# Kernel tuning notes

Hardware: AMD Instinct MI355X
Metric: run time of the kernel (lower is better)

## Reference

```python
import jax, jax.numpy as jnp
import numpy as np

DIM = 32
N_TOKENS = 4
HIDDEN = 2 * DIM
BATCH = 262144
EPS = 1e-5
SCALE = 1.0 / float(np.sqrt(DIM))


def _ln(x, g, b):
    m = jnp.mean(x, axis=-1, keepdims=True)
    v = jnp.mean((x - m) ** 2, axis=-1, keepdims=True)
    return (x - m) * jax.lax.rsqrt(v + EPS) * g + b


def setup_inputs() -> dict:
    key = jax.random.key(0)
    ks = jax.random.split(key, 16)
    s = 0.02
    lin = lambda k, i, o: jax.random.normal(k, (i, o), jnp.float32) * s
    return {
        "x": jax.random.normal(ks[0], (BATCH, N_TOKENS, DIM), jnp.float32),
        "w_pe": lin(ks[1], DIM, DIM),
        "b_pe": jnp.zeros((DIM,), jnp.float32),
        "pos": jax.random.normal(ks[2], (1, N_TOKENS, DIM), jnp.float32) * s,
        "ln1_g": jnp.ones((DIM,), jnp.float32),
        "ln1_b": jnp.zeros((DIM,), jnp.float32),
        "wq": lin(ks[3], DIM, DIM), "bq": jnp.zeros((DIM,), jnp.float32),
        "wk": lin(ks[4], DIM, DIM), "bk": jnp.zeros((DIM,), jnp.float32),
        "wv": lin(ks[5], DIM, DIM), "bv": jnp.zeros((DIM,), jnp.float32),
        "wo": lin(ks[6], DIM, DIM), "bo": jnp.zeros((DIM,), jnp.float32),
        "ln2_g": jnp.ones((DIM,), jnp.float32),
        "ln2_b": jnp.zeros((DIM,), jnp.float32),
        "w1": lin(ks[7], DIM, HIDDEN), "bf1": jnp.zeros((HIDDEN,), jnp.float32),
        "w2": lin(ks[8], HIDDEN, DIM), "bf2": jnp.zeros((DIM,), jnp.float32),
    }


def reference(x, w_pe, b_pe, pos, ln1_g, ln1_b, wq, bq, wk, bk, wv, bv,
              wo, bo, ln2_g, ln2_b, w1, bf1, w2, bf2):
    # patch embed + positional embedding
    x = x @ w_pe + b_pe + pos                      # [B, T, D]
    # attention block
    xa = _ln(x, ln1_g, ln1_b)
    q = xa @ wq + bq
    k = xa @ wk + bk
    v = xa @ wv + bv
    scores = jnp.einsum("btd,bsd->bts", q, k) * SCALE  # [B, T, T]
    attn = jax.nn.softmax(scores, axis=-1)
    mixed = jnp.einsum("bts,bsd->btd", attn, v)
    x = x + mixed @ wo + bo
    # MLP block (gelu tanh approximation, matching F.gelu(approximate='tanh'))
    xb = _ln(x, ln2_g, ln2_b)
    h = jax.nn.gelu(xb @ w1 + bf1, approximate=True)   # [B, T, 2D]
    x = x + h @ w2 + bf2
    return x
```

## Files before the change

### kernel.cpp

```cpp
#include <hip/hip_runtime.h>
#include <hip/hip_bf16.h>

typedef float          f32x4  __attribute__((ext_vector_type(4)));
typedef __bf16         bf16x8 __attribute__((ext_vector_type(8)));
typedef unsigned short u16x8  __attribute__((ext_vector_type(8)));
typedef unsigned int   u32;

#define DEV static __device__ __forceinline__

static constexpr int   NT      = 65536;
static constexpr float SCALE_Q = 0.17677669529663687f;
static constexpr float LOG2E   = 1.44269504f;

DEV unsigned short f2bf(float f) {
  return __builtin_bit_cast(unsigned short, __float2bfloat16(f));
}
DEV u32 pk2(float lo, float hi) { return (u32)f2bf(lo) | ((u32)f2bf(hi) << 16); }

DEV u16x8 pack8(f32x4 a, f32x4 b) {
  uint4 q;
  q.x = pk2(a[0], a[1]); q.y = pk2(a[2], a[3]);
  q.z = pk2(b[0], b[1]); q.w = pk2(b[2], b[3]);
  return __builtin_bit_cast(u16x8, q);
}

DEV f32x4 mfma(u16x8 a, u16x8 b, f32x4 c) {
  return __builtin_amdgcn_mfma_f32_16x16x32_bf16(
      __builtin_bit_cast(bf16x8, a), __builtin_bit_cast(bf16x8, b), c, 0, 0, 0);
}
DEV void wait_lds() {
  asm volatile("s_waitcnt lgkmcnt(0)" ::: "memory");
  __builtin_amdgcn_sched_barrier(0);
}

DEV u16x8 build_frag(const float* W, int N, int k0, int col, float scale) {
  u16x8 f;
#pragma unroll
  for (int e = 0; e < 8; ++e)
    f[e] = f2bf(W[(k0 + e) * N + col] * scale);
  return f;
}
DEV u16x8 fold_frag(u16x8 f, const float* gv) {
  u16x8 o;
#pragma unroll
  for (int e = 0; e < 8; ++e) {
    union { u32 i; float v; } u; u.i = ((u32)f[e]) << 16;
    o[e] = f2bf(u.v * gv[e]);
  }
  return o;
}

DEV u16x8 conv_std(u32* buf, int r15, int lg, f32x4 a0, f32x4 a1) {
  const int wb = r15 * 20 + 2 * lg;
  buf[wb + 0] = pk2(a0[0], a0[1]);
  buf[wb + 1] = pk2(a0[2], a0[3]);
  buf[wb + 8] = pk2(a1[0], a1[1]);
  buf[wb + 9] = pk2(a1[2], a1[3]);
  wait_lds();
  uint4 rd = *(const uint4*)(buf + r15 * 20 + 4 * lg);
  return __builtin_bit_cast(u16x8, rd);
}

DEV void ln_stats(f32x4 a, f32x4 b, float& rs, float& nm) {
  float s1 = 0.f, s2 = 0.f;
#pragma unroll
  for (int i = 0; i < 4; ++i) { s1 += a[i]; s2 = fmaf(a[i], a[i], s2); }
#pragma unroll
  for (int i = 0; i < 4; ++i) { s1 += b[i]; s2 = fmaf(b[i], b[i], s2); }
  s1 += __shfl_xor(s1, 16); s2 += __shfl_xor(s2, 16);
  s1 += __shfl_xor(s1, 32); s2 += __shfl_xor(s2, 32);
  const float m   = s1 * 0.03125f;
  const float var = fmaf(s2, 0.03125f, -m * m);
  rs = __builtin_amdgcn_rsqf(var + 1e-5f);
  nm = -m * rs;
}

DEV float gelu_t(float u) {
  const float u2 = u * u;
  float z2 = u * fmaf(u2, 0.07135481f, 1.59576912f);
  z2 = fminf(z2, 80.f);
  const float e = __builtin_amdgcn_exp2f(z2 * LOG2E);
  return u * e * __builtin_amdgcn_rcpf(e + 1.0f);
}

__global__ __launch_bounds__(256, 2) void vit_fused(
    const float* __restrict__ x,
    const float* __restrict__ wpe, const float* __restrict__ bpe,
    const float* __restrict__ pos,
    const float* __restrict__ ln1g, const float* __restrict__ ln1b,
    const float* __restrict__ wq, const float* __restrict__ bq,
    const float* __restrict__ wk, const float* __restrict__ bk,
    const float* __restrict__ wv, const float* __restrict__ bv,
    const float* __restrict__ wo, const float* __restrict__ bo,
    const float* __restrict__ ln2g, const float* __restrict__ ln2b,
    const float* __restrict__ w1, const float* __restrict__ bf1,
    const float* __restrict__ w2, const float* __restrict__ bf2,
    float* __restrict__ out) {
  const int tid = (int)threadIdx.x;
  const int wid = tid >> 6;
  const int l   = tid & 63;
  const int r15 = l & 15;
  const int lg  = l >> 4;
  const int tk  = l & 3;

  __shared__ alignas(16) u32   s_conv[4][2][320];
  __shared__ alignas(16) float s_q[4][576];
  __shared__ alignas(16) float s_k[4][576];
  __shared__ alignas(16) float s_vv[4][576];
  __shared__ alignas(16) float s_at[4][64];
  __shared__ alignas(16) u32   s_h[4][576];
  u32*   bufA = s_conv[wid][0];
  u32*   bufB = s_conv[wid][1];
  float* qS   = s_q[wid];
  float* kS   = s_k[wid];
  float* vS   = s_vv[wid];
  float* aT   = s_at[wid];
  u32*   hB   = s_h[wid];

  float g1v[8], g2v[8];
#pragma unroll
  for (int e = 0; e < 8; ++e) { g1v[e] = ln1g[8 * lg + e]; g2v[e] = ln2g[8 * lg + e]; }
  const u16x8 b1f = pack8(*(const f32x4*)(ln1b + 8 * lg), *(const f32x4*)(ln1b + 8 * lg + 4));
  const u16x8 b2f = pack8(*(const f32x4*)(ln2b + 8 * lg), *(const f32x4*)(ln2b + 8 * lg + 4));

  u16x8 wpeF[2], wqF[2], wkF[2], wvF[2], woF[2], w1F[4], w2F[2][2];
  f32x4 comboC[2], bqC[2], bkC[2], bvC[2], boC[2], bf2C[2], bf1C[4];

#pragma unroll
  for (int H = 0; H < 2; ++H) {
    const int dc  = 16 * H + 4 * lg;
    const int col = 16 * H + r15;
    wpeF[H]   = build_frag(wpe, 32, 8 * lg, col, 1.f);
    woF[H]    = build_frag(wo,  32, 8 * lg, col, 1.f);
    w2F[0][H] = build_frag(w2,  32, 8 * lg,      col, 1.f);
    w2F[1][H] = build_frag(w2,  32, 32 + 8 * lg, col, 1.f);
    f32x4 cq, ck, cv, cmb, cbo, cb2;
#pragma unroll
    for (int i = 0; i < 4; ++i) {
      const int d = dc + i;
      cmb[i] = bpe[d] + pos[tk * 32 + d];
      cq[i]  = SCALE_Q * bq[d];
      ck[i]  = bk[d];
      cv[i]  = bv[d];
      cbo[i] = bo[d];
      cb2[i] = bf2[d];
    }
    comboC[H] = cmb; boC[H] = cbo; bf2C[H] = cb2;
    const u16x8 rq = build_frag(wq, 32, 8 * lg, col, SCALE_Q);
    const u16x8 rk = build_frag(wk, 32, 8 * lg, col, 1.f);
    const u16x8 rv = build_frag(wv, 32, 8 * lg, col, 1.f);
    bqC[H] = mfma(rq, b1f, cq);
    bkC[H] = mfma(rk, b1f, ck);
    bvC[H] = mfma(rv, b1f, cv);
    wqF[H] = fold_frag(rq, g1v);
    wkF[H] = fold_frag(rk, g1v);
    wvF[H] = fold_frag(rv, g1v);
  }
#pragma unroll
  for (int Hp = 0; Hp < 4; ++Hp) {
    const int col = 16 * Hp + r15;
    const u16x8 r1 = build_frag(w1, 64, 8 * lg, col, 1.f);
    f32x4 c1;
#pragma unroll
    for (int i = 0; i < 4; ++i) c1[i] = bf1[16 * Hp + 4 * lg + i];
    bf1C[Hp] = mfma(r1, b2f, c1);
    w1F[Hp]  = fold_frag(r1, g2v);
  }

  const f32x4 zero4 = {0.f, 0.f, 0.f, 0.f};
  const int stride = (int)(gridDim.x << 2);
  int tile = (int)(blockIdx.x << 2) | wid;

  const float* xp = x + (size_t)(tile * 16 + r15) * 32 + 8 * lg;
  f32x4 xv0 = *(const f32x4*)(xp);
  f32x4 xv1 = *(const f32x4*)(xp + 4);
  for (; tile < NT; tile += stride) {
    const int nxt = tile + stride;
    f32x4 nx0 = xv0, nx1 = xv1;
    if (nxt < NT) {
      const float* np_ = x + (size_t)(nxt * 16 + r15) * 32 + 8 * lg;
      nx0 = *(const f32x4*)(np_);
      nx1 = *(const f32x4*)(np_ + 4);
    }
    const u16x8 xf = pack8(xv0, xv1);

    f32x4 x1a = mfma(wpeF[0], xf, comboC[0]);
    f32x4 x1b = mfma(wpeF[1], xf, comboC[1]);

    float rs, nm;
    ln_stats(x1a, x1b, rs, nm);
    f32x4 ya, yb;
#pragma unroll
    for (int i = 0; i < 4; ++i) { ya[i] = fmaf(x1a[i], rs, nm); yb[i] = fmaf(x1b[i], rs, nm); }
    const u16x8 xaf = conv_std(bufA, r15, lg, ya, yb);

    const f32x4 qa0 = mfma(wqF[0], xaf, bqC[0]);
    const f32x4 qa1 = mfma(wqF[1], xaf, bqC[1]);
    const f32x4 ka0 = mfma(wkF[0], xaf, bkC[0]);
    const f32x4 ka1 = mfma(wkF[1], xaf, bkC[1]);
    const f32x4 va0 = mfma(wvF[0], xaf, bvC[0]);
    const f32x4 va1 = mfma(wvF[1], xaf, bvC[1]);

    *(f32x4*)(qS + r15 * 36 + 4 * lg)      = qa0;
    *(f32x4*)(qS + r15 * 36 + 16 + 4 * lg) = qa1;
    *(f32x4*)(kS + r15 * 36 + 4 * lg)      = ka0;
    *(f32x4*)(kS + r15 * 36 + 16 + 4 * lg) = ka1;
    *(f32x4*)(vS + r15 * 36 + 4 * lg)      = va0;
    *(f32x4*)(vS + r15 * 36 + 16 + 4 * lg) = va1;
    wait_lds();

    const int qr = l >> 2;
    const int kr = (qr & 12) | (l & 3);
    float sc = 0.f;
#pragma unroll
    for (int c = 0; c < 8; ++c) {
      const f32x4 qv = *(const f32x4*)(qS + qr * 36 + 4 * c);
      const f32x4 kv = *(const f32x4*)(kS + kr * 36 + 4 * c);
      sc = fmaf(qv[0], kv[0], sc); sc = fmaf(qv[1], kv[1], sc);
      sc = fmaf(qv[2], kv[2], sc); sc = fmaf(qv[3], kv[3], sc);
    }
    float t0 = fmaxf(sc, __shfl_xor(sc, 1));
    const float mx = fmaxf(t0, __shfl_xor(t0, 2));
    const float ex = __builtin_amdgcn_exp2f((sc - mx) * LOG2E);
    float se = ex + __shfl_xor(ex, 1);
    se = se + __shfl_xor(se, 2);
    aT[l] = ex * __builtin_amdgcn_rcpf(se);
    wait_lds();

    const f32x4 atv = *(const f32x4*)(aT + (r15 << 2));
    f32x4 m0 = zero4, m1 = zero4;
#pragma unroll
    for (int j = 0; j < 4; ++j) {
      const f32x4 v0 = *(const f32x4*)(vS + ((r15 & 12) + j) * 36 + 4 * lg);
      const f32x4 v1 = *(const f32x4*)(vS + ((r15 & 12) + j) * 36 + 16 + 4 * lg);
      m0 += atv[j] * v0;
      m1 += atv[j] * v1;
    }
    const u16x8 mf = conv_std(bufB, r15, lg, m0, m1);

    const f32x4 x2a = mfma(woF[0], mf, x1a) + boC[0];
    const f32x4 x2b = mfma(woF[1], mf, x1b) + boC[1];

    ln_stats(x2a, x2b, rs, nm);
#pragma unroll
    for (int i = 0; i < 4; ++i) { ya[i] = fmaf(x2a[i], rs, nm); yb[i] = fmaf(x2b[i], rs, nm); }
    const u16x8 xbf = conv_std(bufA, r15, lg, ya, yb);

#pragma unroll
    for (int Hp = 0; Hp < 4; ++Hp) {
      const f32x4 h = mfma(w1F[Hp], xbf, bf1C[Hp]);
      const int hb = r15 * 36 + 8 * Hp + 2 * lg;
      hB[hb]     = pk2(gelu_t(h[0]), gelu_t(h[1]));
      hB[hb + 1] = pk2(gelu_t(h[2]), gelu_t(h[3]));
    }
    wait_lds();
    const uint4 h0r = *(const uint4*)(hB + r15 * 36 + 4 * lg);
    const uint4 h1r = *(const uint4*)(hB + r15 * 36 + 16 + 4 * lg);
    const u16x8 hf0 = __builtin_bit_cast(u16x8, h0r);
    const u16x8 hf1 = __builtin_bit_cast(u16x8, h1r);

    f32x4 o0 = x2a + bf2C[0];
    f32x4 o1 = x2b + bf2C[1];
    o0 = mfma(w2F[0][0], hf0, o0);
    o0 = mfma(w2F[1][0], hf1, o0);
    o1 = mfma(w2F[0][1], hf0, o1);
    o1 = mfma(w2F[1][1], hf1, o1);

    float* op = out + (size_t)(tile * 16 + r15) * 32;
    *(f32x4*)(op + 4 * lg)      = o0;
    *(f32x4*)(op + 16 + 4 * lg) = o1;

    xv0 = nx0; xv1 = nx1;
  }
}

extern "C" void kernel_launch(void* const* d_in, const int* in_sizes, int n_in,
                              void* d_out, int out_size, void* d_ws, size_t ws_size,
                              hipStream_t stream) {
  (void)in_sizes; (void)n_in; (void)d_ws; (void)ws_size; (void)out_size;
  const float* x    = (const float*)d_in[0];
  const float* wpe  = (const float*)d_in[1];
  const float* bpe  = (const float*)d_in[2];
  const float* pos  = (const float*)d_in[3];
  const float* ln1g = (const float*)d_in[4];
  const float* ln1b = (const float*)d_in[5];
  const float* wq   = (const float*)d_in[6];
  const float* bq   = (const float*)d_in[7];
  const float* wk   = (const float*)d_in[8];
  const float* bk   = (const float*)d_in[9];
  const float* wv   = (const float*)d_in[10];
  const float* bv   = (const float*)d_in[11];
  const float* wo   = (const float*)d_in[12];
  const float* bo   = (const float*)d_in[13];
  const float* ln2g = (const float*)d_in[14];
  const float* ln2b = (const float*)d_in[15];
  const float* w1   = (const float*)d_in[16];
  const float* bf1  = (const float*)d_in[17];
  const float* w2   = (const float*)d_in[18];
  const float* bf2  = (const float*)d_in[19];

  vit_fused<<<512, 256, 0, stream>>>(x, wpe, bpe, pos, ln1g, ln1b, wq, bq, wk, bk,
                                     wv, bv, wo, bo, ln2g, ln2b, w1, bf1, w2, bf2,
                                     (float*)d_out);
}
```

Baseline: 93.44 us.

## Compute attention scores with MFMA and shrink LDS to raise occupancy

Q and K are converted to bf16 fragments through the LDS conversion buffers, and the 16x16 score tile comes from one MFMA instead of scalar FMA dot products over fp32 LDS copies. Softmax over each 4-token group now runs in registers without cross-lane shuffles. The q/k LDS arrays are dropped, V and the hidden buffer share one array, launch bounds go to 4 blocks per CU, and the grid doubles to 1024 blocks. Scores are now computed in bf16 rather than fp32, which costs some precision, and the higher occupancy target may push registers toward spilling.

```diff
diff --git a/kernel.cpp b/kernel.cpp
--- a/kernel.cpp
+++ b/kernel.cpp
@@ -61,6 +61,23 @@
   return __builtin_bit_cast(u16x8, rd);
 }
 
+DEV void conv_qk(u32* bq_, u32* bk_, int r15, int lg,
+                 f32x4 q0, f32x4 q1, f32x4 k0, f32x4 k1,
+                 u16x8& qf, u16x8& kf) {
+  const int wb = r15 * 20 + 2 * lg;
+  bq_[wb + 0] = pk2(q0[0], q0[1]);
+  bq_[wb + 1] = pk2(q0[2], q0[3]);
+  bq_[wb + 8] = pk2(q1[0], q1[1]);
+  bq_[wb + 9] = pk2(q1[2], q1[3]);
+  bk_[wb + 0] = pk2(k0[0], k0[1]);
+  bk_[wb + 1] = pk2(k0[2], k0[3]);
+  bk_[wb + 8] = pk2(k1[0], k1[1]);
+  bk_[wb + 9] = pk2(k1[2], k1[3]);
+  wait_lds();
+  qf = __builtin_bit_cast(u16x8, *(const uint4*)(bq_ + r15 * 20 + 4 * lg));
+  kf = __builtin_bit_cast(u16x8, *(const uint4*)(bk_ + r15 * 20 + 4 * lg));
+}
+
 DEV void ln_stats(f32x4 a, f32x4 b, float& rs, float& nm) {
   float s1 = 0.f, s2 = 0.f;
 #pragma unroll
@@ -83,7 +100,7 @@
   return u * e * __builtin_amdgcn_rcpf(e + 1.0f);
 }
 
-__global__ __launch_bounds__(256, 2) void vit_fused(
+__global__ __launch_bounds__(256, 4) void vit_fused(
     const float* __restrict__ x,
     const float* __restrict__ wpe, const float* __restrict__ bpe,
     const float* __restrict__ pos,
@@ -104,18 +121,13 @@
   const int tk  = l & 3;
 
   __shared__ alignas(16) u32   s_conv[4][2][320];
-  __shared__ alignas(16) float s_q[4][576];
-  __shared__ alignas(16) float s_k[4][576];
-  __shared__ alignas(16) float s_vv[4][576];
+  __shared__ alignas(16) float s_vh[4][576];
   __shared__ alignas(16) float s_at[4][64];
-  __shared__ alignas(16) u32   s_h[4][576];
   u32*   bufA = s_conv[wid][0];
   u32*   bufB = s_conv[wid][1];
-  float* qS   = s_q[wid];
-  float* kS   = s_k[wid];
-  float* vS   = s_vv[wid];
+  float* vS   = s_vh[wid];
+  u32*   hB   = (u32*)s_vh[wid];
   float* aT   = s_at[wid];
-  u32*   hB   = s_h[wid];
 
   float g1v[8], g2v[8];
 #pragma unroll
@@ -201,33 +213,26 @@
     const f32x4 va0 = mfma(wvF[0], xaf, bvC[0]);
     const f32x4 va1 = mfma(wvF[1], xaf, bvC[1]);
 
-    *(f32x4*)(qS + r15 * 36 + 4 * lg)      = qa0;
-    *(f32x4*)(qS + r15 * 36 + 16 + 4 * lg) = qa1;
-    *(f32x4*)(kS + r15 * 36 + 4 * lg)      = ka0;
-    *(f32x4*)(kS + r15 * 36 + 16 + 4 * lg) = ka1;
     *(f32x4*)(vS + r15 * 36 + 4 * lg)      = va0;
     *(f32x4*)(vS + r15 * 36 + 16 + 4 * lg) = va1;
+
+    u16x8 qf, kf;
+    conv_qk(bufB, bufA, r15, lg, qa0, qa1, ka0, ka1, qf, kf);
+
+    const f32x4 sc = mfma(kf, qf, zero4);
+    {
+      const float mx = fmaxf(fmaxf(sc[0], sc[1]), fmaxf(sc[2], sc[3]));
+      const float e0 = __builtin_amdgcn_exp2f((sc[0] - mx) * LOG2E);
+      const float e1 = __builtin_amdgcn_exp2f((sc[1] - mx) * LOG2E);
+      const float e2 = __builtin_amdgcn_exp2f((sc[2] - mx) * LOG2E);
+      const float e3 = __builtin_amdgcn_exp2f((sc[3] - mx) * LOG2E);
+      const float rc = __builtin_amdgcn_rcpf((e0 + e1) + (e2 + e3));
+      f32x4 p; p[0] = e0 * rc; p[1] = e1 * rc; p[2] = e2 * rc; p[3] = e3 * rc;
+      if (lg == (r15 >> 2)) *(f32x4*)(aT + 4 * r15) = p;
+    }
     wait_lds();
 
-    const int qr = l >> 2;
-    const int kr = (qr & 12) | (l & 3);
-    float sc = 0.f;
-#pragma unroll
-    for (int c = 0; c < 8; ++c) {
-      const f32x4 qv = *(const f32x4*)(qS + qr * 36 + 4 * c);
-      const f32x4 kv = *(const f32x4*)(kS + kr * 36 + 4 * c);
-      sc = fmaf(qv[0], kv[0], sc); sc = fmaf(qv[1], kv[1], sc);
-      sc = fmaf(qv[2], kv[2], sc); sc = fmaf(qv[3], kv[3], sc);
-    }
-    float t0 = fmaxf(sc, __shfl_xor(sc, 1));
-    const float mx = fmaxf(t0, __shfl_xor(t0, 2));
-    const float ex = __builtin_amdgcn_exp2f((sc - mx) * LOG2E);
-    float se = ex + __shfl_xor(ex, 1);
-    se = se + __shfl_xor(se, 2);
-    aT[l] = ex * __builtin_amdgcn_rcpf(se);
-    wait_lds();
-
-    const f32x4 atv = *(const f32x4*)(aT + (r15 << 2));
+    const f32x4 atv = *(const f32x4*)(aT + 4 * r15);
     f32x4 m0 = zero4, m1 = zero4;
 #pragma unroll
     for (int j = 0; j < 4; ++j) {
@@ -299,7 +304,7 @@
   const float* w2   = (const float*)d_in[18];
   const float* bf2  = (const float*)d_in[19];
 
-  vit_fused<<<512, 256, 0, stream>>>(x, wpe, bpe, pos, ln1g, ln1b, wq, bq, wk, bk,
-                                     wv, bv, wo, bo, ln2g, ln2b, w1, bf1, w2, bf2,
-                                     (float*)d_out);
-}
+  vit_fused<<<1024, 256, 0, stream>>>(x, wpe, bpe, pos, ln1g, ln1b, wq, bq, wk, bk,
+                                      wv, bv, wo, bo, ln2g, ln2b, w1, bf1, w2, bf2,
+                                      (float*)d_out);
+}
```

Measured after the change: 211.2 us. +126.0%, slower.
